# Kernel optimization log

Hardware: AMD Instinct MI355X
Metric: run time of the kernel (lower is better)

Reference implementation:

```python
import jax, jax.numpy as jnp
import numpy as np
from jax import lax


def _sobel_kernels(angle_deg, channel_n):
    dx = np.outer([1.0, 2.0, 1.0], [-1.0, 0.0, 1.0]) / 8.0
    dy = dx.T
    c = np.cos(angle_deg * np.pi / 180.0)
    s = np.sin(angle_deg * np.pi / 180.0)
    w1 = (c * dx - s * dy).astype(np.float32)
    w2 = (s * dx + c * dy).astype(np.float32)
    # depthwise kernels [C, 1, 3, 3] (OIHW with feature_group_count=C)
    k1 = jnp.tile(jnp.asarray(w1)[None, None], (channel_n, 1, 1, 1))
    k2 = jnp.tile(jnp.asarray(w2)[None, None], (channel_n, 1, 1, 1))
    return k1, k2


def _dwconv(x, k, groups):
    return lax.conv_general_dilated(
        x, k, window_strides=(1, 1), padding=[(1, 1), (1, 1)],
        feature_group_count=groups,
        dimension_numbers=('NCHW', 'OIHW', 'NCHW'))


def _maxpool3(x):
    # 3x3 max pool, stride 1, pad 1 over last two dims of NCHW
    return lax.reduce_window(x, -jnp.inf, lax.max,
                             (1, 1, 3, 3), (1, 1, 1, 1),
                             [(0, 0), (0, 0), (1, 1), (1, 1)])


def _alive(x_nchw):
    return _maxpool3(x_nchw[:, 3:4]) > 0.1


def _update(x, key, w0, b0, w1, wfr, k1, k2):
    # x: [B, H, W, C]  (torch does transpose(1,3) -> [B, C, W, H])
    xc = jnp.swapaxes(x, 1, 3)
    pre = _alive(xc)                               # [B,1,W,H] bool
    cn = xc.shape[1]
    y1 = _dwconv(xc, k1, cn)
    y2 = _dwconv(xc, k2, cn)
    dx = jnp.swapaxes(jnp.concatenate([xc, y1, y2], axis=1), 1, 3)  # [B,H,W,3C]
    fr = jax.nn.sigmoid(dx @ wfr.T) * jnp.swapaxes(pre, 1, 3)       # [B,H,W,1]
    log_fr = jnp.log(jnp.concatenate([fr, 1.0 - fr], axis=-1) + 1e-10)
    h = jax.nn.relu(dx @ w0.T + b0) @ w1.T                           # [B,H,W,C]
    # gumbel-softmax, tau=1, hard=True (straight-through)
    u = jax.random.uniform(key, log_fr.shape)
    g = -jnp.log(-jnp.log(u + 1e-20) + 1e-20)
    soft = jax.nn.softmax(log_fr + g, axis=-1)
    hard = jax.nn.one_hot(jnp.argmax(soft, axis=-1), 2, dtype=soft.dtype)
    update_grid = (hard + soft - lax.stop_gradient(soft))[..., 0:1]
    h = h * update_grid
    xc = xc + jnp.swapaxes(h, 1, 3)
    post = _alive(xc)
    xc = xc * (pre & post).astype(xc.dtype)
    return jnp.swapaxes(xc, 1, 3), fr[..., 0]


def setup_inputs() -> dict:
    key = jax.random.key(0)
    k = jax.random.split(key, 5)
    B, H, W, C, HID = 16, 128, 128, 16, 256
    return {
        'x': jax.random.uniform(k[0], (B, H, W, C), dtype=jnp.float32),
        'w0': jax.random.normal(k[1], (HID, 3 * C), dtype=jnp.float32) * 0.1,
        'b0': jax.random.normal(k[2], (HID,), dtype=jnp.float32) * 0.01,
        'w1': jax.random.normal(k[3], (C, HID), dtype=jnp.float32) * 0.1,
        'wfr': jax.random.normal(k[4], (1, 3 * C), dtype=jnp.float32) * 0.1,
        'steps': 4,
    }


def reference(x, w0, b0, w1, wfr, steps):
    angle = 0.0
    k1, k2 = _sobel_kernels(angle, x.shape[-1])
    keys = jax.random.split(jax.random.key(42), steps)

    def step(carry, key):
        xn, fr = _update(carry, key, w0, b0, w1, wfr, k1, k2)
        return xn, (xn, fr)

    _, (x_steps, fr_steps) = lax.scan(step, x, keys)
    return x_steps, fr_steps
```

## Files before the change

kernel.cpp:

```cpp
#include <hip/hip_runtime.h>
#include <cstdint>
#include <math.h>

#define HW2    16384
#define BHW    262144
#define XSLICE 4194304

__host__ __device__ static inline uint32_t rotl32(uint32_t v, int r) {
  return (v << r) | (v >> (32 - r));
}

__host__ __device__ static inline void tf2x32(uint32_t k0, uint32_t k1,
                                              uint32_t x0, uint32_t x1,
                                              uint32_t& o0, uint32_t& o1) {
  uint32_t ks2 = k0 ^ k1 ^ 0x1BD11BDAu;
  x0 += k0; x1 += k1;
#define TFR(r) { x0 += x1; x1 = rotl32(x1, (r)); x1 ^= x0; }
  TFR(13) TFR(15) TFR(26) TFR(6)   x0 += k1;  x1 += ks2 + 1u;
  TFR(17) TFR(29) TFR(16) TFR(24)  x0 += ks2; x1 += k0 + 2u;
  TFR(13) TFR(15) TFR(26) TFR(6)   x0 += k0;  x1 += k1 + 3u;
  TFR(17) TFR(29) TFR(16) TFR(24)  x0 += k1;  x1 += ks2 + 4u;
  TFR(13) TFR(15) TFR(26) TFR(6)   x0 += ks2; x1 += k0 + 5u;
#undef TFR
  o0 = x0; o1 = x1;
}

__device__ static inline float bits_to_unit(uint32_t bits) {
  return __uint_as_float((bits >> 9) | 0x3f800000u) - 1.0f;
}

__device__ static inline uint32_t rng_bits(uint32_t sk0, uint32_t sk1, uint32_t f) {
  uint32_t o0, o1;
  tf2x32(sk0, sk1, 0u, f, o0, o1);
  return o0 ^ o1;
}

__device__ static inline float sigmoidf_(float z) {
  if (z >= 0.f) { float e = expf(-z); return 1.f / (1.f + e); }
  float e = expf(z); return e / (1.f + e);
}

__device__ static inline void sobel_feat(const float* __restrict__ base,
                                         int hh, int ww, float* dxv, float& m3) {
#pragma unroll
  for (int c = 0; c < 48; ++c) dxv[c] = 0.f;
  m3 = -INFINITY;
#pragma unroll
  for (int dh = -1; dh <= 1; ++dh) {
    const int j = dh + 1;
    const int h2 = hh + dh;
    const bool hok = ((unsigned)h2 < 128u);
#pragma unroll
    for (int dw = -1; dw <= 1; ++dw) {
      const int i = dw + 1;
      const int w2 = ww + dw;
      float v[16];
      if (hok && ((unsigned)w2 < 128u)) {
        const float* s = base + (((h2 << 7) + w2) << 4);
#pragma unroll
        for (int c = 0; c < 16; c += 4) {
          float4 q = *(const float4*)(s + c);
          v[c] = q.x; v[c + 1] = q.y; v[c + 2] = q.z; v[c + 3] = q.w;
        }
        m3 = fmaxf(m3, v[3]);
      } else {
#pragma unroll
        for (int c = 0; c < 16; ++c) v[c] = 0.f;
      }
      const float smv[3] = {1.f, 2.f, 1.f};
      const float dfv[3] = {-1.f, 0.f, 1.f};
      const float c1 = smv[i] * dfv[j] * 0.125f;
      const float c2 = dfv[i] * smv[j] * 0.125f;
      if (dh == 0 && dw == 0) {
#pragma unroll
        for (int c = 0; c < 16; ++c) dxv[c] = v[c];
      }
      if (c1 != 0.f) {
#pragma unroll
        for (int c = 0; c < 16; ++c) dxv[16 + c] = fmaf(c1, v[c], dxv[16 + c]);
      }
      if (c2 != 0.f) {
#pragma unroll
        for (int c = 0; c < 16; ++c) dxv[32 + c] = fmaf(c2, v[c], dxv[32 + c]);
      }
    }
  }
}

__global__ __launch_bounds__(256, 2) void ca_step_a(
    const float* __restrict__ xin,
    const float* __restrict__ w0g,
    const float* __restrict__ b0g,
    const float* __restrict__ w1g,
    const float* __restrict__ wfrg,
    float* __restrict__ xmid,
    float* __restrict__ ch3,
    float* __restrict__ premask,
    float* __restrict__ frout,
    uint32_t sk0, uint32_t sk1) {
  __shared__ float sw[128 * 68];

  const int tid = threadIdx.x;
  const int p0  = blockIdx.x * 512 + tid;
  const int p1  = p0 + 256;
  const int b   = p0 >> 14;
  const int rem = p0 & 16383;
  const int hh0 = rem >> 7;
  const int ww0 = rem & 127;
  const int hh1 = hh0 + 2;

  const float* base = xin + ((size_t)b << 18);

  float dx0[48], dx1[48];
  float m30, m31;
  sobel_feat(base, hh0, ww0, dx0, m30);
  sobel_feat(base, hh1, ww0, dx1, m31);

  const bool pre0 = (m30 > 0.1f);
  const bool pre1 = (m31 > 0.1f);

  float z0 = 0.f, z1 = 0.f;
#pragma unroll
  for (int c = 0; c < 48; ++c) {
    z0 = fmaf(dx0[c], wfrg[c], z0);
    z1 = fmaf(dx1[c], wfrg[c], z1);
  }
  const float fr0 = pre0 ? sigmoidf_(z0) : 0.f;
  const float fr1 = pre1 ? sigmoidf_(z1) : 0.f;

  float upd0, upd1;
  {
    const float u0 = bits_to_unit(rng_bits(sk0, sk1, 2u * (uint32_t)p0));
    const float u1 = bits_to_unit(rng_bits(sk0, sk1, 2u * (uint32_t)p0 + 1u));
    const float d0 = logf(fr0 + 1e-10f) - logf(-logf(u0 + 1e-20f) + 1e-20f);
    const float d1 = logf(1.0f - fr0 + 1e-10f) - logf(-logf(u1 + 1e-20f) + 1e-20f);
    upd0 = (d0 >= d1) ? 1.f : 0.f;
  }
  {
    const float u0 = bits_to_unit(rng_bits(sk0, sk1, 2u * (uint32_t)p1));
    const float u1 = bits_to_unit(rng_bits(sk0, sk1, 2u * (uint32_t)p1 + 1u));
    const float d0 = logf(fr1 + 1e-10f) - logf(-logf(u0 + 1e-20f) + 1e-20f);
    const float d1 = logf(1.0f - fr1 + 1e-10f) - logf(-logf(u1 + 1e-20f) + 1e-20f);
    upd1 = (d0 >= d1) ? 1.f : 0.f;
  }

  float h0[16], h1[16];
#pragma unroll
  for (int c = 0; c < 16; ++c) { h0[c] = 0.f; h1[c] = 0.f; }

  for (int pass = 0; pass < 2; ++pass) {
    const int jb = pass << 7;
    if (pass) __syncthreads();
    {
      const float4* w04 = (const float4*)w0g;
      float4* sw4 = (float4*)sw;
      for (int i = tid; i < 1536; i += 256) {
        const int j = i / 12, q = i - j * 12;
        sw4[j * 17 + q] = w04[(jb + j) * 12 + q];
      }
      if (tid < 128) sw[tid * 68 + 48] = b0g[jb + tid];
      for (int i = tid; i < 2048; i += 256) {
        const int j = i & 127, c = i >> 7;
        sw[j * 68 + 52 + c] = w1g[c * 256 + jb + j];
      }
    }
    __syncthreads();
#pragma unroll 2
    for (int jj = 0; jj < 128; ++jj) {
      const float* row = sw + jj * 68;
      float a00 = 0.f, a01 = 0.f, a10 = 0.f, a11 = 0.f;
#pragma unroll
      for (int k = 0; k < 48; k += 8) {
        const float4 wa = *(const float4*)(row + k);
        const float4 wb = *(const float4*)(row + k + 4);
        a00 = fmaf(wa.x, dx0[k + 0], a00); a01 = fmaf(wa.y, dx0[k + 1], a01);
        a00 = fmaf(wa.z, dx0[k + 2], a00); a01 = fmaf(wa.w, dx0[k + 3], a01);
        a00 = fmaf(wb.x, dx0[k + 4], a00); a01 = fmaf(wb.y, dx0[k + 5], a01);
        a00 = fmaf(wb.z, dx0[k + 6], a00); a01 = fmaf(wb.w, dx0[k + 7], a01);
        a10 = fmaf(wa.x, dx1[k + 0], a10); a11 = fmaf(wa.y, dx1[k + 1], a11);
        a10 = fmaf(wa.z, dx1[k + 2], a10); a11 = fmaf(wa.w, dx1[k + 3], a11);
        a10 = fmaf(wb.x, dx1[k + 4], a10); a11 = fmaf(wb.y, dx1[k + 5], a11);
        a10 = fmaf(wb.z, dx1[k + 6], a10); a11 = fmaf(wb.w, dx1[k + 7], a11);
      }
      const float bb = row[48];
      const float r0 = fmaxf(bb + (a00 + a01), 0.f);
      const float r1 = fmaxf(bb + (a10 + a11), 0.f);
#pragma unroll
      for (int c = 0; c < 16; c += 4) {
        const float4 q = *(const float4*)(row + 52 + c);
        h0[c]     = fmaf(q.x, r0, h0[c]);     h1[c]     = fmaf(q.x, r1, h1[c]);
        h0[c + 1] = fmaf(q.y, r0, h0[c + 1]); h1[c + 1] = fmaf(q.y, r1, h1[c + 1]);
        h0[c + 2] = fmaf(q.z, r0, h0[c + 2]); h1[c + 2] = fmaf(q.z, r1, h1[c + 2]);
        h0[c + 3] = fmaf(q.w, r0, h0[c + 3]); h1[c + 3] = fmaf(q.w, r1, h1[c + 3]);
      }
    }
  }

  float* dst0 = xmid + ((size_t)p0 << 4);
  float* dst1 = xmid + ((size_t)p1 << 4);
#pragma unroll
  for (int c = 0; c < 16; c += 4) {
    float4 q0, q1;
    q0.x = fmaf(upd0, h0[c],     dx0[c]);     q1.x = fmaf(upd1, h1[c],     dx1[c]);
    q0.y = fmaf(upd0, h0[c + 1], dx0[c + 1]); q1.y = fmaf(upd1, h1[c + 1], dx1[c + 1]);
    q0.z = fmaf(upd0, h0[c + 2], dx0[c + 2]); q1.z = fmaf(upd1, h1[c + 2], dx1[c + 2]);
    q0.w = fmaf(upd0, h0[c + 3], dx0[c + 3]); q1.w = fmaf(upd1, h1[c + 3], dx1[c + 3]);
    *(float4*)(dst0 + c) = q0;
    *(float4*)(dst1 + c) = q1;
  }
  ch3[p0]     = fmaf(upd0, h0[3], dx0[3]);
  ch3[p1]     = fmaf(upd1, h1[3], dx1[3]);
  premask[p0] = pre0 ? 1.f : 0.f;
  premask[p1] = pre1 ? 1.f : 0.f;
  frout[p0]   = fr0;
  frout[p1]   = fr1;
}

__global__ __launch_bounds__(256) void ca_step_b(
    float* __restrict__ xs, const float* __restrict__ ch3,
    const float* __restrict__ premask) {
  const int p   = blockIdx.x * 256 + threadIdx.x;
  const int b   = p >> 14;
  const int rem = p & 16383;
  const int hh  = rem >> 7;
  const int ww  = rem & 127;
  const float* cb = ch3 + (b << 14);
  float m = -INFINITY;
#pragma unroll
  for (int dh = -1; dh <= 1; ++dh) {
    const int h2 = hh + dh;
    if ((unsigned)h2 >= 128u) continue;
#pragma unroll
    for (int dw = -1; dw <= 1; ++dw) {
      const int w2 = ww + dw;
      if ((unsigned)w2 >= 128u) continue;
      m = fmaxf(m, cb[(h2 << 7) + w2]);
    }
  }
  const bool alive = (premask[p] != 0.f) && (m > 0.1f);
  if (!alive) {
    float4 z; z.x = 0.f; z.y = 0.f; z.z = 0.f; z.w = 0.f;
    float* dst = xs + ((size_t)p << 4);
    *(float4*)(dst)      = z;
    *(float4*)(dst + 4)  = z;
    *(float4*)(dst + 8)  = z;
    *(float4*)(dst + 12) = z;
  }
}

extern "C" void kernel_launch(void* const* d_in, const int* in_sizes, int n_in,
                              void* d_out, int out_size, void* d_ws, size_t ws_size,
                              hipStream_t stream) {
  const float* x0  = (const float*)d_in[0];
  const float* w0  = (const float*)d_in[1];
  const float* b0  = (const float*)d_in[2];
  const float* w1  = (const float*)d_in[3];
  const float* wfr = (const float*)d_in[4];
  const int steps = 4;

  float* xsteps  = (float*)d_out;
  float* frsteps = xsteps + (size_t)steps * XSLICE;

  float* ch3 = (float*)d_ws;
  float* pre = ch3 + BHW;

  uint32_t sk[4][2];
  for (int s = 0; s < steps; ++s)
    tf2x32(0u, 42u, 0u, (uint32_t)s, sk[s][0], sk[s][1]);

  for (int s = 0; s < steps; ++s) {
    const float* xin = (s == 0) ? x0 : (xsteps + (size_t)(s - 1) * XSLICE);
    float* xmid = xsteps + (size_t)s * XSLICE;
    ca_step_a<<<512, 256, 0, stream>>>(xin, w0, b0, w1, wfr, xmid, ch3, pre,
                                       frsteps + (size_t)s * BHW, sk[s][0], sk[s][1]);
    ca_step_b<<<1024, 256, 0, stream>>>(xmid, ch3, pre);
  }
}
```

Measured before the change: 505.1 us.

## Pre-pack MLP weights once and split hidden units between LDS and scalar loads

A one-time pack kernel builds a contiguous weight table in workspace, with each hidden unit's w0 row, its transposed w1 column and its bias together. ca_step_a now copies only the first 128 hidden units into shared memory with a single bulk copy and sync, replacing the two strided per-pass staging loops. The other 128 units are read straight from global memory with uniform addresses, so they can be served as scalar/constant loads. This removes the second sync and staging pass and mixes LDS and scalar-cache reads, but adds register pressure from the 65-float per-row array and depends on uniform global loads being cheap.

```diff
diff --git a/kernel.cpp b/kernel.cpp
--- a/kernel.cpp
+++ b/kernel.cpp
@@ -89,9 +89,7 @@
 
 __global__ __launch_bounds__(256, 2) void ca_step_a(
     const float* __restrict__ xin,
-    const float* __restrict__ w0g,
-    const float* __restrict__ b0g,
-    const float* __restrict__ w1g,
+    const float* __restrict__ pw,
     const float* __restrict__ wfrg,
     float* __restrict__ xmid,
     float* __restrict__ ch3,
@@ -101,6 +99,13 @@
   __shared__ float sw[128 * 68];
 
   const int tid = threadIdx.x;
+  {
+    const float4* src = (const float4*)pw;
+    float4* dst = (float4*)sw;
+    for (int i = tid; i < 2176; i += 256) dst[i] = src[i];
+  }
+  __syncthreads();
+
   const int p0  = blockIdx.x * 512 + tid;
   const int p1  = p0 + 256;
   const int b   = p0 >> 14;
@@ -148,29 +153,18 @@
 #pragma unroll
   for (int c = 0; c < 16; ++c) { h0[c] = 0.f; h1[c] = 0.f; }
 
-  for (int pass = 0; pass < 2; ++pass) {
-    const int jb = pass << 7;
-    if (pass) __syncthreads();
+  for (int i = 0; i < 128; ++i) {
+    const float* __restrict__ srow = pw + (size_t)(128 + i) * 68;
+    float S[65];
+#pragma unroll
+    for (int q = 0; q < 65; ++q) S[q] = srow[q];
+
     {
-      const float4* w04 = (const float4*)w0g;
-      float4* sw4 = (float4*)sw;
-      for (int i = tid; i < 1536; i += 256) {
-        const int j = i / 12, q = i - j * 12;
-        sw4[j * 17 + q] = w04[(jb + j) * 12 + q];
-      }
-      if (tid < 128) sw[tid * 68 + 48] = b0g[jb + tid];
-      for (int i = tid; i < 2048; i += 256) {
-        const int j = i & 127, c = i >> 7;
-        sw[j * 68 + 52 + c] = w1g[c * 256 + jb + j];
-      }
-    }
-    __syncthreads();
-#pragma unroll 2
-    for (int jj = 0; jj < 128; ++jj) {
-      const float* row = sw + jj * 68;
+      const float* row = sw + i * 68;
       float a00 = 0.f, a01 = 0.f, a10 = 0.f, a11 = 0.f;
 #pragma unroll
-      for (int k = 0; k < 48; k += 8) {
+      for (int ks = 0; ks < 6; ++ks) {
+        const int k = ks * 8;
         const float4 wa = *(const float4*)(row + k);
         const float4 wb = *(const float4*)(row + k + 4);
         a00 = fmaf(wa.x, dx0[k + 0], a00); a01 = fmaf(wa.y, dx0[k + 1], a01);
@@ -182,16 +176,34 @@
         a10 = fmaf(wb.x, dx1[k + 4], a10); a11 = fmaf(wb.y, dx1[k + 5], a11);
         a10 = fmaf(wb.z, dx1[k + 6], a10); a11 = fmaf(wb.w, dx1[k + 7], a11);
       }
-      const float bb = row[48];
+      const float bb = row[64];
       const float r0 = fmaxf(bb + (a00 + a01), 0.f);
       const float r1 = fmaxf(bb + (a10 + a11), 0.f);
 #pragma unroll
-      for (int c = 0; c < 16; c += 4) {
-        const float4 q = *(const float4*)(row + 52 + c);
+      for (int c4 = 0; c4 < 4; ++c4) {
+        const float4 q = *(const float4*)(row + 48 + (c4 << 2));
+        const int c = c4 << 2;
         h0[c]     = fmaf(q.x, r0, h0[c]);     h1[c]     = fmaf(q.x, r1, h1[c]);
         h0[c + 1] = fmaf(q.y, r0, h0[c + 1]); h1[c + 1] = fmaf(q.y, r1, h1[c + 1]);
         h0[c + 2] = fmaf(q.z, r0, h0[c + 2]); h1[c + 2] = fmaf(q.z, r1, h1[c + 2]);
         h0[c + 3] = fmaf(q.w, r0, h0[c + 3]); h1[c + 3] = fmaf(q.w, r1, h1[c + 3]);
+      }
+    }
+
+    {
+      float a00 = 0.f, a01 = 0.f, a10 = 0.f, a11 = 0.f;
+#pragma unroll
+      for (int k = 0; k < 48; k += 2) {
+        a00 = fmaf(S[k], dx0[k], a00);     a01 = fmaf(S[k + 1], dx0[k + 1], a01);
+        a10 = fmaf(S[k], dx1[k], a10);     a11 = fmaf(S[k + 1], dx1[k + 1], a11);
+      }
+      const float bb = S[64];
+      const float r0 = fmaxf(bb + (a00 + a01), 0.f);
+      const float r1 = fmaxf(bb + (a10 + a11), 0.f);
+#pragma unroll
+      for (int c = 0; c < 16; ++c) {
+        h0[c] = fmaf(S[48 + c], r0, h0[c]);
+        h1[c] = fmaf(S[48 + c], r1, h1[c]);
       }
     }
   }
@@ -248,6 +260,22 @@
   }
 }
 
+__global__ void pack_weights(const float* __restrict__ w0,
+                             const float* __restrict__ b0,
+                             const float* __restrict__ w1,
+                             float* __restrict__ pw) {
+  const int j = blockIdx.x * 256 + threadIdx.x;
+  if (j < 256) {
+    float* r = pw + j * 68;
+#pragma unroll
+    for (int k = 0; k < 48; ++k) r[k] = w0[j * 48 + k];
+#pragma unroll
+    for (int c = 0; c < 16; ++c) r[48 + c] = w1[c * 256 + j];
+    r[64] = b0[j];
+    r[65] = 0.f; r[66] = 0.f; r[67] = 0.f;
+  }
+}
+
 extern "C" void kernel_launch(void* const* d_in, const int* in_sizes, int n_in,
                               void* d_out, int out_size, void* d_ws, size_t ws_size,
                               hipStream_t stream) {
@@ -261,17 +289,19 @@
   float* xsteps  = (float*)d_out;
   float* frsteps = xsteps + (size_t)steps * XSLICE;
 
-  float* ch3 = (float*)d_ws;
+  float* pw  = (float*)d_ws;
+  float* ch3 = pw + 17408;
   float* pre = ch3 + BHW;
 
   uint32_t sk[4][2];
   for (int s = 0; s < steps; ++s)
     tf2x32(0u, 42u, 0u, (uint32_t)s, sk[s][0], sk[s][1]);
 
+  pack_weights<<<1, 256, 0, stream>>>(w0, b0, w1, pw);
   for (int s = 0; s < steps; ++s) {
     const float* xin = (s == 0) ? x0 : (xsteps + (size_t)(s - 1) * XSLICE);
     float* xmid = xsteps + (size_t)s * XSLICE;
-    ca_step_a<<<512, 256, 0, stream>>>(xin, w0, b0, w1, wfr, xmid, ch3, pre,
+    ca_step_a<<<512, 256, 0, stream>>>(xin, pw, wfr, xmid, ch3, pre,
                                        frsteps + (size_t)s * BHW, sk[s][0], sk[s][1]);
     ca_step_b<<<1024, 256, 0, stream>>>(xmid, ch3, pre);
   }
```

Result: faster. 462.8 us (-8.4%).
